# Kernel tuning notes

Hardware: AMD Instinct MI355X
Metric: run time of the kernel (lower is better)

The kernel has to match this reference:

```python
import jax, jax.numpy as jnp
import numpy as np

N_NODES = 200000
NNZ = 6400000
EMBED_DIM = 128


def setup_inputs() -> dict:
    key = jax.random.key(0)
    k1, k2, k3, k4 = jax.random.split(key, 4)
    ego_embeddings = jax.random.normal(k1, (N_NODES, EMBED_DIM), dtype=jnp.float32)
    adj_values = jax.random.uniform(k2, (NNZ,), dtype=jnp.float32)
    row_idx = jax.random.randint(k3, (NNZ,), 0, N_NODES, dtype=jnp.int32)
    col_idx = jax.random.randint(k4, (NNZ,), 0, N_NODES, dtype=jnp.int32)
    return {
        "ego_embeddings": ego_embeddings,
        "adj_values": adj_values,
        "row_idx": row_idx,
        "col_idx": col_idx,
    }


def reference(ego_embeddings, adj_values, row_idx, col_idx):
    # SpMM: out[r] = sum over nnz with row==r of adj_values * ego_embeddings[col]
    # == tf.sparse.sparse_dense_matmul(adj_mat, ego_embeddings)
    messages = adj_values[:, None] * ego_embeddings[col_idx]  # [nnz, D]
    out = jax.ops.segment_sum(messages, row_idx, num_segments=N_NODES)
    return out
```

## Files before the change

### kernel.cpp

```cpp
#include <hip/hip_runtime.h>
#include <hip/hip_fp16.h>


constexpr int D     = 128;
constexpr int RPB   = 256;
constexpr int CAP   = 9728;
constexpr int LDSB  = 3 * 256 * 4 + CAP * 8;
constexpr int CTILE = 8192;
constexpr int STILE = 16384;

__global__ void __launch_bounds__(256)
ego_to_h(const float* __restrict__ src, __half* __restrict__ dst, int n8) {
    int i = blockIdx.x * 256 + threadIdx.x;
    if (i >= n8) return;
    const float4* s4 = (const float4*)src;
    float4 a = s4[2 * i], b = s4[2 * i + 1];
    __half2 h0 = __floats2half2_rn(a.x, a.y);
    __half2 h1 = __floats2half2_rn(a.z, a.w);
    __half2 h2 = __floats2half2_rn(b.x, b.y);
    __half2 h3 = __floats2half2_rn(b.z, b.w);
    uint4 o;
    o.x = *(unsigned int*)&h0;
    o.y = *(unsigned int*)&h1;
    o.z = *(unsigned int*)&h2;
    o.w = *(unsigned int*)&h3;
    ((uint4*)dst)[i] = o;
}

__global__ void __launch_bounds__(256)
coarse_count(const int* __restrict__ rows, int* __restrict__ bcnt, int nnz) {
    __shared__ int h[1024];
    int tid = threadIdx.x;
    for (int i = tid; i < 1024; i += 256) h[i] = 0;
    __syncthreads();
    int base = blockIdx.x * CTILE;
    int cnt = min(CTILE, nnz - base);
    for (int i = tid; i < cnt; i += 256)
        atomicAdd(&h[rows[base + i] >> 8], 1);
    __syncthreads();
    for (int i = tid; i < 1024; i += 256)
        if (h[i]) atomicAdd(&bcnt[i], h[i]);
}

__global__ void __launch_bounds__(1024)
scan_buckets(const int* __restrict__ bcnt, int* __restrict__ bbase,
             int* __restrict__ bcursor) {
    __shared__ int s[1024];
    int tid = threadIdx.x;
    int v = bcnt[tid];
    s[tid] = v;
    __syncthreads();
    for (int off = 1; off < 1024; off <<= 1) {
        int t = (tid >= off) ? s[tid - off] : 0;
        __syncthreads();
        s[tid] += t;
        __syncthreads();
    }
    int ex = s[tid] - v;
    bbase[tid] = ex;
    bcursor[tid] = ex;
    if (tid == 1023) bbase[1024] = s[tid];
}

__global__ void __launch_bounds__(1024)
coarse_scatter(const int* __restrict__ rows, const int* __restrict__ cols,
               const float* __restrict__ vals, int* __restrict__ bcursor,
               int2* __restrict__ pairs, int nnz) {
    __shared__ int h[1024], sc[1024], cur[1024], gb[1024];
    __shared__ unsigned short src[STILE];
    int tid = threadIdx.x;
    h[tid] = 0;
    __syncthreads();
    int base = blockIdx.x * STILE;
    int cnt = min(STILE, nnz - base);
    for (int i = tid; i < cnt; i += 1024)
        atomicAdd(&h[rows[base + i] >> 8], 1);
    __syncthreads();
    int v = h[tid];
    sc[tid] = v;
    __syncthreads();
    for (int off = 1; off < 1024; off <<= 1) {
        int t = (tid >= off) ? sc[tid - off] : 0;
        __syncthreads();
        sc[tid] += t;
        __syncthreads();
    }
    int excl = sc[tid] - v;
    cur[tid] = excl;
    if (v) gb[tid] = atomicAdd(&bcursor[tid], v) - excl;
    __syncthreads();
    for (int i = tid; i < cnt; i += 1024) {
        int b = rows[base + i] >> 8;
        int slot = atomicAdd(&cur[b], 1);
        src[slot] = (unsigned short)i;
    }
    __syncthreads();
    for (int s_ = tid; s_ < cnt; s_ += 1024) {
        int e = src[s_];
        int r = rows[base + e];
        int c = cols[base + e];
        float vv = vals[base + e];
        pairs[gb[r >> 8] + s_] = make_int2(((r & 255) << 18) | c, __float_as_int(vv));
    }
}

__global__ void __launch_bounds__(1024)
bucket_gather(const int* __restrict__ bbase, const int2* __restrict__ pairs,
              const __half* __restrict__ egoh, float* __restrict__ out, int N) {
    extern __shared__ int smem[];
    int* h   = smem;
    int* sS  = smem + 256;
    int* cur = smem + 512;
    int2* lp = (int2*)(smem + 768);
    int b = blockIdx.x, tid = threadIdx.x;
    int start = bbase[b], end = bbase[b + 1];
    int wid = tid >> 6, lane = tid & 63;
    int total = end - start;
    int nch = (total + CAP - 1) / CAP;
    if (nch == 0 && (b << 8) < N) nch = 1;
    for (int ch = 0; ch < nch; ++ch) {
        int cbase = start + ch * CAP;
        int ccnt  = min(CAP, end - cbase);
        if (ccnt < 0) ccnt = 0;
        if (tid < 256) h[tid] = 0;
        __syncthreads();
        for (int i = tid; i < ccnt; i += 1024)
            atomicAdd(&h[(unsigned)pairs[cbase + i].x >> 18], 1);
        __syncthreads();
        if (tid < 256) sS[tid] = h[tid];
        __syncthreads();
        for (int off = 1; off < 256; off <<= 1) {
            int t = 0;
            if (tid < 256 && tid >= off) t = sS[tid - off];
            __syncthreads();
            if (tid < 256) sS[tid] += t;
            __syncthreads();
        }
        if (tid < 256) {
            int e = sS[tid] - h[tid];
            sS[tid] = e;
            cur[tid] = e;
        }
        __syncthreads();
        for (int i = tid; i < ccnt; i += 1024) {
            int2 p = pairs[cbase + i];
            int pos = atomicAdd(&cur[(unsigned)p.x >> 18], 1);
            lp[pos] = p;
        }
        __syncthreads();
        for (int ri = 0; ri < 16; ++ri) {
            int lr  = wid * 16 + ri;
            int s0  = sS[lr];
            int sen = s0 + h[lr];
            float2 acc = {0.f, 0.f};
            for (int bb = s0; bb < sen; bb += 64) {
                int j = bb + lane;
                int cvx = 0, cvy = 0;
                if (j < sen) {
                    int2 p = lp[j];
                    cvx = p.x;
                    cvy = p.y;
                }
                int m_ = min(64, sen - bb);
                int k = 0;
                for (; k + 8 <= m_; k += 8) {
                    int c0 = __builtin_amdgcn_readlane(cvx, k + 0) & 0x3FFFF;
                    int c1 = __builtin_amdgcn_readlane(cvx, k + 1) & 0x3FFFF;
                    int c2 = __builtin_amdgcn_readlane(cvx, k + 2) & 0x3FFFF;
                    int c3 = __builtin_amdgcn_readlane(cvx, k + 3) & 0x3FFFF;
                    int c4 = __builtin_amdgcn_readlane(cvx, k + 4) & 0x3FFFF;
                    int c5 = __builtin_amdgcn_readlane(cvx, k + 5) & 0x3FFFF;
                    int c6 = __builtin_amdgcn_readlane(cvx, k + 6) & 0x3FFFF;
                    int c7 = __builtin_amdgcn_readlane(cvx, k + 7) & 0x3FFFF;
                    float v0 = __int_as_float(__builtin_amdgcn_readlane(cvy, k + 0));
                    float v1 = __int_as_float(__builtin_amdgcn_readlane(cvy, k + 1));
                    float v2 = __int_as_float(__builtin_amdgcn_readlane(cvy, k + 2));
                    float v3 = __int_as_float(__builtin_amdgcn_readlane(cvy, k + 3));
                    float v4 = __int_as_float(__builtin_amdgcn_readlane(cvy, k + 4));
                    float v5 = __int_as_float(__builtin_amdgcn_readlane(cvy, k + 5));
                    float v6 = __int_as_float(__builtin_amdgcn_readlane(cvy, k + 6));
                    float v7 = __int_as_float(__builtin_amdgcn_readlane(cvy, k + 7));
                    __half2 e0 = ((const __half2*)(egoh + (size_t)c0 * D))[lane];
                    __half2 e1 = ((const __half2*)(egoh + (size_t)c1 * D))[lane];
                    __half2 e2 = ((const __half2*)(egoh + (size_t)c2 * D))[lane];
                    __half2 e3 = ((const __half2*)(egoh + (size_t)c3 * D))[lane];
                    __half2 e4 = ((const __half2*)(egoh + (size_t)c4 * D))[lane];
                    __half2 e5 = ((const __half2*)(egoh + (size_t)c5 * D))[lane];
                    __half2 e6 = ((const __half2*)(egoh + (size_t)c6 * D))[lane];
                    __half2 e7 = ((const __half2*)(egoh + (size_t)c7 * D))[lane];
                    float2 f0 = __half22float2(e0);
                    float2 f1 = __half22float2(e1);
                    float2 f2 = __half22float2(e2);
                    float2 f3 = __half22float2(e3);
                    float2 f4 = __half22float2(e4);
                    float2 f5 = __half22float2(e5);
                    float2 f6 = __half22float2(e6);
                    float2 f7 = __half22float2(e7);
                    acc.x += v0 * f0.x; acc.y += v0 * f0.y;
                    acc.x += v1 * f1.x; acc.y += v1 * f1.y;
                    acc.x += v2 * f2.x; acc.y += v2 * f2.y;
                    acc.x += v3 * f3.x; acc.y += v3 * f3.y;
                    acc.x += v4 * f4.x; acc.y += v4 * f4.y;
                    acc.x += v5 * f5.x; acc.y += v5 * f5.y;
                    acc.x += v6 * f6.x; acc.y += v6 * f6.y;
                    acc.x += v7 * f7.x; acc.y += v7 * f7.y;
                }
                for (; k < m_; ++k) {
                    int   c = __builtin_amdgcn_readlane(cvx, k) & 0x3FFFF;
                    float v = __int_as_float(__builtin_amdgcn_readlane(cvy, k));
                    __half2 e = ((const __half2*)(egoh + (size_t)c * D))[lane];
                    float2 f = __half22float2(e);
                    acc.x += v * f.x;
                    acc.y += v * f.y;
                }
            }
            int grow = (b << 8) + lr;
            if (grow < N) {
                float2* dst = (float2*)(out + (size_t)grow * D) + lane;
                if (nch > 1 && ch > 0) {
                    float2 pv = *dst;
                    acc.x += pv.x;
                    acc.y += pv.y;
                }
                *dst = acc;
            }
        }
        __syncthreads();
    }
}

__global__ void __launch_bounds__(256)
spmm_scatter(const float* __restrict__ vals, const int* __restrict__ rows,
             const int* __restrict__ cols, const float* __restrict__ ego,
             float* __restrict__ out, int nnz) {
    int edge = (blockIdx.x * blockDim.x + threadIdx.x) >> 6;
    int lane = threadIdx.x & 63;
    if (edge >= nnz) return;
    int   r = __builtin_amdgcn_readfirstlane(rows[edge]);
    int   c = __builtin_amdgcn_readfirstlane(cols[edge]);
    float v = vals[edge];
    float2 m = ((const float2*)(ego + (size_t)c * D))[lane];
    float* dst = out + (size_t)r * D + 2 * lane;
    unsafeAtomicAdd(dst,     v * m.x);
    unsafeAtomicAdd(dst + 1, v * m.y);
}

extern "C" void kernel_launch(void* const* d_in, const int* in_sizes, int n_in,
                              void* d_out, int out_size, void* d_ws, size_t ws_size,
                              hipStream_t stream) {
    const float* ego  = (const float*)d_in[0];
    const float* vals = (const float*)d_in[1];
    const int*   rows = (const int*)d_in[2];
    const int*   cols = (const int*)d_in[3];
    float*       out  = (float*)d_out;
    int nnz = in_sizes[1];
    int N   = out_size / D;
    int nb  = (N + RPB - 1) / RPB;

    static int attr_ok = -1;
    if (attr_ok < 0) {
        attr_ok = (hipFuncSetAttribute(
                       reinterpret_cast<const void*>(bucket_gather),
                       hipFuncAttributeMaxDynamicSharedMemorySize,
                       LDSB) == hipSuccess)
                      ? 1 : 0;
    }

    size_t need = (size_t)4096 * 4 + (size_t)nnz * 8 + (size_t)N * D * 2;
    if (ws_size < need || N > 262144 || nb > 1024 || !attr_ok) {
        hipMemsetAsync(d_out, 0, (size_t)out_size * sizeof(float), stream);
        spmm_scatter<<<(nnz + 3) / 4, 256, 0, stream>>>(vals, rows, cols, ego, out, nnz);
        return;
    }

    int* ws      = (int*)d_ws;
    int* bcnt    = ws;
    int* bbase   = ws + 1024;
    int* bcursor = ws + 3072;
    int2* pairs  = (int2*)(ws + 4096);
    __half* egoh = (__half*)(pairs + nnz);

    int ntc = (nnz + CTILE - 1) / CTILE;
    int nts = (nnz + STILE - 1) / STILE;
    int n8  = N * D / 8;

    hipMemsetAsync(bcnt, 0, 1024 * sizeof(int), stream);
    ego_to_h      <<<(n8 + 255) / 256, 256, 0, stream>>>(ego, egoh, n8);
    coarse_count  <<<ntc, 256, 0, stream>>>(rows, bcnt, nnz);
    scan_buckets  <<<1, 1024, 0, stream>>>(bcnt, bbase, bcursor);
    coarse_scatter<<<nts, 1024, 0, stream>>>(rows, cols, vals, bcursor, pairs, nnz);
    bucket_gather <<<nb, 1024, LDSB, stream>>>(bbase, pairs, egoh, out, N);
}
```

Before: 669.1 us.

## Use wave-shuffle block scans and register-staged single-pass reads in binning kernels

Replaces the shared-memory Hillis-Steele scans, which take many barriers, with a wave-shuffle two-level block scan in scan_buckets, coarse_scatter and bucket_gather. coarse_scatter now loads rows, cols and vals once into registers, bins the packed entries into LDS, and has each thread write its bucket's contiguous run out to global memory. It no longer re-reads global memory through an index array. bucket_gather likewise keeps its chunk of pairs in registers so the chunk is read once instead of twice. In exchange the scatter tile is halved, which doubles block count and bucket-cursor atomics, register pressure rises, and the per-thread bucket writes are less coalesced.

```diff
diff --git a/kernel.cpp b/kernel.cpp
--- a/kernel.cpp
+++ b/kernel.cpp
@@ -5,9 +5,33 @@
 constexpr int D     = 128;
 constexpr int RPB   = 256;
 constexpr int CAP   = 9728;
-constexpr int LDSB  = 3 * 256 * 4 + CAP * 8;
+constexpr int GLDS  = 3 * 256 * 4 + CAP * 8;
+constexpr int SLDS  = 4 * 1024 * 4 + 8192 * 8;
 constexpr int CTILE = 8192;
-constexpr int STILE = 16384;
+constexpr int STILE = 8192;
+
+__device__ __forceinline__ int block_scan_1024(int v, int* wsum, int tid) {
+    int lane = tid & 63, w = tid >> 6;
+    int s = v;
+    #pragma unroll
+    for (int off = 1; off < 64; off <<= 1) {
+        int t = __shfl_up(s, off, 64);
+        if (lane >= off) s += t;
+    }
+    if (lane == 63) wsum[w] = s;
+    __syncthreads();
+    if (w == 0) {
+        int ws = (lane < 16) ? wsum[lane] : 0;
+        #pragma unroll
+        for (int off = 1; off < 16; off <<= 1) {
+            int t = __shfl_up(ws, off, 64);
+            if (lane >= off) ws += t;
+        }
+        if (lane < 16) wsum[lane] = ws;
+    }
+    __syncthreads();
+    return s + ((w > 0) ? wsum[w - 1] : 0);
+}
 
 __global__ void __launch_bounds__(256)
 ego_to_h(const float* __restrict__ src, __half* __restrict__ dst, int n8) {
@@ -45,63 +69,66 @@
 __global__ void __launch_bounds__(1024)
 scan_buckets(const int* __restrict__ bcnt, int* __restrict__ bbase,
              int* __restrict__ bcursor) {
-    __shared__ int s[1024];
+    __shared__ int wsum[17];
     int tid = threadIdx.x;
     int v = bcnt[tid];
-    s[tid] = v;
-    __syncthreads();
-    for (int off = 1; off < 1024; off <<= 1) {
-        int t = (tid >= off) ? s[tid - off] : 0;
-        __syncthreads();
-        s[tid] += t;
-        __syncthreads();
-    }
-    int ex = s[tid] - v;
+    int incl = block_scan_1024(v, wsum, tid);
+    int ex = incl - v;
     bbase[tid] = ex;
     bcursor[tid] = ex;
-    if (tid == 1023) bbase[1024] = s[tid];
+    if (tid == 1023) bbase[1024] = incl;
 }
 
 __global__ void __launch_bounds__(1024)
 coarse_scatter(const int* __restrict__ rows, const int* __restrict__ cols,
                const float* __restrict__ vals, int* __restrict__ bcursor,
                int2* __restrict__ pairs, int nnz) {
-    __shared__ int h[1024], sc[1024], cur[1024], gb[1024];
-    __shared__ unsigned short src[STILE];
+    extern __shared__ int smem[];
+    int*   h    = smem;
+    int*   sS   = smem + 1024;
+    int*   cur  = smem + 2048;
+    int*   gb   = smem + 3072;
+    int*   lcol = smem + 4096;
+    float* lval = (float*)(smem + 4096 + STILE);
     int tid = threadIdx.x;
-    h[tid] = 0;
-    __syncthreads();
     int base = blockIdx.x * STILE;
     int cnt = min(STILE, nnz - base);
-    for (int i = tid; i < cnt; i += 1024)
-        atomicAdd(&h[rows[base + i] >> 8], 1);
+    h[tid] = 0;
+    __syncthreads();
+    int pc[8], pb[8];
+    float pv[8];
+    #pragma unroll
+    for (int j = 0; j < 8; ++j) {
+        int i = tid + j * 1024;
+        pb[j] = -1;
+        if (i < cnt) {
+            int r = rows[base + i], c = cols[base + i];
+            pv[j] = vals[base + i];
+            pb[j] = r >> 8;
+            pc[j] = ((r & 255) << 18) | c;
+            atomicAdd(&h[pb[j]], 1);
+        }
+    }
     __syncthreads();
     int v = h[tid];
-    sc[tid] = v;
-    __syncthreads();
-    for (int off = 1; off < 1024; off <<= 1) {
-        int t = (tid >= off) ? sc[tid - off] : 0;
-        __syncthreads();
-        sc[tid] += t;
-        __syncthreads();
-    }
-    int excl = sc[tid] - v;
-    cur[tid] = excl;
-    if (v) gb[tid] = atomicAdd(&bcursor[tid], v) - excl;
-    __syncthreads();
-    for (int i = tid; i < cnt; i += 1024) {
-        int b = rows[base + i] >> 8;
-        int slot = atomicAdd(&cur[b], 1);
-        src[slot] = (unsigned short)i;
-    }
-    __syncthreads();
-    for (int s_ = tid; s_ < cnt; s_ += 1024) {
-        int e = src[s_];
-        int r = rows[base + e];
-        int c = cols[base + e];
-        float vv = vals[base + e];
-        pairs[gb[r >> 8] + s_] = make_int2(((r & 255) << 18) | c, __float_as_int(vv));
-    }
+    int incl = block_scan_1024(v, gb , tid);
+    __syncthreads();
+    int ex = incl - v;
+    sS[tid] = ex;
+    cur[tid] = ex;
+    if (v) gb[tid] = atomicAdd(&bcursor[tid], v);
+    __syncthreads();
+    #pragma unroll
+    for (int j = 0; j < 8; ++j)
+        if (pb[j] >= 0) {
+            int slot = atomicAdd(&cur[pb[j]], 1);
+            lcol[slot] = pc[j];
+            lval[slot] = pv[j];
+        }
+    __syncthreads();
+    int s0 = sS[tid], g0 = gb[tid];
+    for (int i = 0; i < v; ++i)
+        pairs[g0 + i] = make_int2(lcol[s0 + i], __float_as_int(lval[s0 + i]));
 }
 
 __global__ void __launch_bounds__(1024)
@@ -124,29 +151,34 @@
         if (ccnt < 0) ccnt = 0;
         if (tid < 256) h[tid] = 0;
         __syncthreads();
-        for (int i = tid; i < ccnt; i += 1024)
-            atomicAdd(&h[(unsigned)pairs[cbase + i].x >> 18], 1);
-        __syncthreads();
-        if (tid < 256) sS[tid] = h[tid];
-        __syncthreads();
-        for (int off = 1; off < 256; off <<= 1) {
-            int t = 0;
-            if (tid < 256 && tid >= off) t = sS[tid - off];
-            __syncthreads();
-            if (tid < 256) sS[tid] += t;
-            __syncthreads();
-        }
+        int px[10], py[10];
+        #pragma unroll
+        for (int j = 0; j < 10; ++j) {
+            int i = tid + j * 1024;
+            px[j] = -1;
+            if (i < ccnt) {
+                int2 p = pairs[cbase + i];
+                px[j] = p.x;
+                py[j] = p.y;
+                atomicAdd(&h[(unsigned)p.x >> 18], 1);
+            }
+        }
+        __syncthreads();
+        int v = (tid < 256) ? h[tid] : 0;
+        int incl = block_scan_1024(v, cur , tid);
+        __syncthreads();
         if (tid < 256) {
-            int e = sS[tid] - h[tid];
+            int e = incl - v;
             sS[tid] = e;
             cur[tid] = e;
         }
         __syncthreads();
-        for (int i = tid; i < ccnt; i += 1024) {
-            int2 p = pairs[cbase + i];
-            int pos = atomicAdd(&cur[(unsigned)p.x >> 18], 1);
-            lp[pos] = p;
-        }
+        #pragma unroll
+        for (int j = 0; j < 10; ++j)
+            if (px[j] >= 0) {
+                int pos = atomicAdd(&cur[(unsigned)px[j] >> 18], 1);
+                lp[pos] = make_int2(px[j], py[j]);
+            }
         __syncthreads();
         for (int ri = 0; ri < 16; ++ri) {
             int lr  = wid * 16 + ri;
@@ -207,11 +239,11 @@
                 }
                 for (; k < m_; ++k) {
                     int   c = __builtin_amdgcn_readlane(cvx, k) & 0x3FFFF;
-                    float v = __int_as_float(__builtin_amdgcn_readlane(cvy, k));
+                    float v_ = __int_as_float(__builtin_amdgcn_readlane(cvy, k));
                     __half2 e = ((const __half2*)(egoh + (size_t)c * D))[lane];
                     float2 f = __half22float2(e);
-                    acc.x += v * f.x;
-                    acc.y += v * f.y;
+                    acc.x += v_ * f.x;
+                    acc.y += v_ * f.y;
                 }
             }
             int grow = (b << 8) + lr;
@@ -259,11 +291,13 @@
 
     static int attr_ok = -1;
     if (attr_ok < 0) {
-        attr_ok = (hipFuncSetAttribute(
-                       reinterpret_cast<const void*>(bucket_gather),
-                       hipFuncAttributeMaxDynamicSharedMemorySize,
-                       LDSB) == hipSuccess)
-                      ? 1 : 0;
+        int ok1 = hipFuncSetAttribute(
+                      reinterpret_cast<const void*>(bucket_gather),
+                      hipFuncAttributeMaxDynamicSharedMemorySize, GLDS) == hipSuccess;
+        int ok2 = hipFuncSetAttribute(
+                      reinterpret_cast<const void*>(coarse_scatter),
+                      hipFuncAttributeMaxDynamicSharedMemorySize, SLDS) == hipSuccess;
+        attr_ok = ok1 && ok2;
     }
 
     size_t need = (size_t)4096 * 4 + (size_t)nnz * 8 + (size_t)N * D * 2;
@@ -288,6 +322,6 @@
     ego_to_h      <<<(n8 + 255) / 256, 256, 0, stream>>>(ego, egoh, n8);
     coarse_count  <<<ntc, 256, 0, stream>>>(rows, bcnt, nnz);
     scan_buckets  <<<1, 1024, 0, stream>>>(bcnt, bbase, bcursor);
-    coarse_scatter<<<nts, 1024, 0, stream>>>(rows, cols, vals, bcursor, pairs, nnz);
-    bucket_gather <<<nb, 1024, LDSB, stream>>>(bbase, pairs, egoh, out, N);
-}
+    coarse_scatter<<<nts, 1024, SLDS, stream>>>(rows, cols, vals, bcursor, pairs, nnz);
+    bucket_gather <<<nb, 1024, GLDS, stream>>>(bbase, pairs, egoh, out, N);
+}
```

Result: faster. 556.3 us (-16.9%).
